# Optimization experiments

Hardware: AMD Instinct MI355X
Metric: run time of the kernel (lower is better)

The kernel has to match this reference:

```python
import jax, jax.numpy as jnp
import numpy as np

E, H = 1024, 16
HD = E // H
QLEN, KLEN, BS = 1024, 2048, 4
PREV = KLEN - QLEN


def _rel_shift(x):
    # x: (q, k, b, h) -> Transformer-XL relative shift
    q, k, b, h = x.shape
    x = jnp.pad(x, ((0, 0), (1, 0), (0, 0), (0, 0)))  # (q, k+1, b, h)
    x = x.reshape(k + 1, q, b, h)[1:].reshape(q, k, b, h)
    return x


def setup_inputs() -> dict:
    key = jax.random.key(0)
    ks = jax.random.split(key, 16)
    s = 0.02  # weight init scale
    inp = {
        "query": jax.random.normal(ks[0], (QLEN, BS, E), jnp.float32),
        "key": jax.random.normal(ks[1], (KLEN, BS, E), jnp.float32),
        "value": jax.random.normal(ks[2], (KLEN, BS, E), jnp.float32),
        "pos_embedding": jax.random.normal(ks[3], (KLEN, 1, E), jnp.float32),
        "U": jax.random.normal(ks[4], (H, HD), jnp.float32) * s,
        "V": jax.random.normal(ks[5], (H, HD), jnp.float32) * s,
        "Wq": jax.random.normal(ks[6], (E, E), jnp.float32) * s,
        "bq": jnp.zeros((E,), jnp.float32),
        "Wk": jax.random.normal(ks[7], (E, E), jnp.float32) * s,
        "bk": jnp.zeros((E,), jnp.float32),
        "Wv": jax.random.normal(ks[8], (E, E), jnp.float32) * s,
        "bv": jnp.zeros((E,), jnp.float32),
        "Wp": jax.random.normal(ks[9], (E, E), jnp.float32) * s,
        "Wo": jax.random.normal(ks[10], (E, E), jnp.float32) * s,
        "bo": jnp.zeros((E,), jnp.float32),
    }
    # causal XL mask: query i attends to keys j <= i + PREV; True = masked
    qi = jnp.arange(QLEN)[:, None]
    kj = jnp.arange(KLEN)[None, :]
    inp["mask"] = (kj > qi + PREV)[:, :, None]  # (q, k, 1) bool
    return inp


def reference(query, key, value, pos_embedding, U, V, Wq, bq, Wk, bk, Wv, bv, Wp, Wo, bo, mask):
    q_len, b, e = query.shape
    k_len = key.shape[0]
    scale = float(np.sqrt(e))  # note: sqrt(embed_dim), as in the source

    queries = (query @ Wq + bq).reshape(q_len, b, H, HD)
    keys = (key @ Wk + bk).reshape(k_len, b, H, HD)
    values = (value @ Wv + bv).reshape(k_len, b, H, HD)
    R = (pos_embedding @ Wp).reshape(-1, H, HD)  # (k, H, HD)

    content_score = jnp.einsum('qbhd,kbhd->qkbh', queries + U, keys)
    position_score = jnp.einsum('qbhd,khd->qkbh', queries + V, R)
    position_score = _rel_shift(position_score)

    attention_score = (content_score + position_score) / scale
    attention_score = jnp.where(mask[..., None], jnp.float32(-1e20), attention_score)
    attention = jax.nn.softmax(attention_score, axis=1)

    alpha = jnp.einsum('qkbh,kbhd->qbhd', attention, values).reshape(q_len, b, e)
    return alpha @ Wo + bo
```

## Files before the change

### kernel.cpp

```cpp
#include <hip/hip_runtime.h>
#include <stdint.h>

#define QLEN 1024
#define KLEN 2048
#define BSZ  4
#define NH   16
#define HD   64
#define EMB  1024
#define PREVL 1024
#define SLOG2E 0.045084220027780106f

typedef __attribute__((ext_vector_type(4))) float f32x4;
typedef __attribute__((ext_vector_type(8))) short bf16x8;

__device__ __forceinline__ unsigned short f2bf(float f){
  unsigned u = __float_as_uint(f);
  u += 0x7fffu + ((u >> 16) & 1u);
  return (unsigned short)(u >> 16);
}

__device__ __forceinline__ void gload_lds16(const void* g, void* l){
  __builtin_amdgcn_global_load_lds((const __attribute__((address_space(1))) void*)g,
                                   (__attribute__((address_space(3))) void*)l, 16, 0, 0);
}

__global__ void txl_prep(const float* __restrict__ w0, const float* __restrict__ w1,
                         const float* __restrict__ w2, const float* __restrict__ w3,
                         const float* __restrict__ w4,
                         unsigned short* __restrict__ o0, unsigned short* __restrict__ o1,
                         unsigned short* __restrict__ o2, unsigned short* __restrict__ o3,
                         unsigned short* __restrict__ o4,
                         const float* __restrict__ q, const float* __restrict__ k,
                         const float* __restrict__ v, const float* __restrict__ p,
                         unsigned short* __restrict__ qo, unsigned short* __restrict__ ko,
                         unsigned short* __restrict__ vo, unsigned short* __restrict__ po){
  const int bid = blockIdx.x;
  if (bid < 5120){
    const int z = bid >> 10, rem = bid & 1023;
    const int by = rem >> 5, bx = rem & 31;
    const float* in; unsigned short* out;
    switch (z){
      case 0: in = w0; out = o0; break;
      case 1: in = w1; out = o1; break;
      case 2: in = w2; out = o2; break;
      case 3: in = w3; out = o3; break;
      default: in = w4; out = o4; break;
    }
    __shared__ float tile[32][33];
    int tx = threadIdx.x & 31, ty = threadIdx.x >> 5;
    int k0 = by * 32, n0 = bx * 32;
    #pragma unroll
    for (int j = 0; j < 32; j += 8)
      tile[ty + j][tx] = in[(size_t)(k0 + ty + j) * EMB + n0 + tx];
    __syncthreads();
    #pragma unroll
    for (int j = 0; j < 32; j += 8)
      out[(size_t)(n0 + ty + j) * EMB + k0 + tx] = f2bf(tile[tx][ty + j]);
  } else {
    for (size_t c = (size_t)(bid - 5120) * 256 + threadIdx.x; c < 2883584; c += (size_t)2048 * 256){
      const float* src; unsigned short* dst; size_t off;
      if (c < 524288)      { src = q; dst = qo; off = c; }
      else if (c < 1572864){ src = k; dst = ko; off = c - 524288; }
      else if (c < 2621440){ src = v; dst = vo; off = c - 1572864; }
      else                 { src = p; dst = po; off = c - 2621440; }
      f32x4 a = *(const f32x4*)(src + off * 8);
      f32x4 b = *(const f32x4*)(src + off * 8 + 4);
      bf16x8 r;
      #pragma unroll
      for (int u = 0; u < 4; ++u){ r[u] = (short)f2bf(a[u]); r[u + 4] = (short)f2bf(b[u]); }
      *(bf16x8*)(dst + off * 8) = r;
    }
  }
}

__global__ __launch_bounds__(256)
void txl_gemm_proj(const unsigned short* __restrict__ pbf, const unsigned short* __restrict__ qbf,
                   const unsigned short* __restrict__ kbf, const unsigned short* __restrict__ vbf,
                   const unsigned short* __restrict__ WpT, const unsigned short* __restrict__ WqT,
                   const unsigned short* __restrict__ WkT, const unsigned short* __restrict__ WvT,
                   const float* __restrict__ bq, const float* __restrict__ bk,
                   const float* __restrict__ bv, const float* __restrict__ U,
                   const float* __restrict__ V,
                   unsigned short* __restrict__ Rb, unsigned short* __restrict__ Qu,
                   unsigned short* __restrict__ Qv, unsigned short* __restrict__ Kb,
                   unsigned short* __restrict__ Vt){
  const int bid = blockIdx.x;
  int mode, local;
  const unsigned short *Ag, *Wt;
  if (bid < 128)      { mode = 3; local = bid;       Ag = pbf; Wt = WpT; }
  else if (bid < 384) { mode = 0; local = bid - 128; Ag = qbf; Wt = WqT; }
  else if (bid < 896) { mode = 1; local = bid - 384; Ag = kbf; Wt = WkT; }
  else                { mode = 2; local = bid - 896; Ag = vbf; Wt = WvT; }
  const int m0 = (local >> 3) * 128, n0 = (local & 7) * 128;

  const int tid = threadIdx.x;
  const int lane = tid & 63, wave = tid >> 6;
  const int lr = lane & 15, lg = lane >> 4;
  const int wm = wave >> 1, wn = wave & 1;
  __shared__ union {
    struct { unsigned short At[128 * 64]; unsigned short Bt[128 * 64]; } ab;
    unsigned short tr[64 * 136];
  } smem;
  unsigned short* At = smem.ab.At;
  unsigned short* Bt = smem.ab.Bt;
  f32x4 acc[4][4] = {};

  for (int kt = 0; kt < EMB / 64; ++kt){
    const int k0 = kt * 64;
    __syncthreads();
    #pragma unroll
    for (int j = 0; j < 4; ++j){
      int row = j * 32 + (tid >> 3);
      int g = (tid & 7) ^ (row & 7);
      gload_lds16(Ag + (size_t)(m0 + row) * EMB + k0 + g * 8, &At[j * 2048 + wave * 512]);
      gload_lds16(Wt + (size_t)(n0 + row) * EMB + k0 + g * 8, &Bt[j * 2048 + wave * 512]);
    }
    __syncthreads();
    #pragma unroll
    for (int ks = 0; ks < 2; ++ks){
      bf16x8 af[4], bfr[4];
      #pragma unroll
      for (int mb = 0; mb < 4; ++mb){
        int row = wm * 64 + mb * 16 + lr;
        af[mb] = *(const bf16x8*)&At[row * 64 + ((lg + 4 * ks) ^ (row & 7)) * 8];
      }
      #pragma unroll
      for (int nb = 0; nb < 4; ++nb){
        int row = wn * 64 + nb * 16 + lr;
        bfr[nb] = *(const bf16x8*)&Bt[row * 64 + ((lg + 4 * ks) ^ (row & 7)) * 8];
      }
      __builtin_amdgcn_s_setprio(1);
      #pragma unroll
      for (int mb = 0; mb < 4; ++mb)
        #pragma unroll
        for (int nb = 0; nb < 4; ++nb)
          acc[mb][nb] = __builtin_amdgcn_mfma_f32_16x16x32_bf16(af[mb], bfr[nb], acc[mb][nb], 0, 0, 0);
      __builtin_amdgcn_s_setprio(0);
    }
  }

  if (mode == 2){
    const int kp0 = m0 >> 2;
    __syncthreads();
    #pragma unroll
    for (int pass = 0; pass < 2; ++pass){
      if (wn == pass){
        #pragma unroll
        for (int mb = 0; mb < 4; ++mb){
          int kp_l = wm * 16 + mb * 4 + lg;
          #pragma unroll
          for (int nb = 0; nb < 4; ++nb){
            int nl = nb * 16 + lr;
            float bvv = bv[n0 + pass * 64 + nl];
            #pragma unroll
            for (int i = 0; i < 4; ++i)
              smem.tr[nl * 136 + i * 32 + kp_l] = f2bf(acc[mb][nb][i] + bvv);
          }
        }
      }
      __syncthreads();
      #pragma unroll
      for (int it = 0; it < 4; ++it){
        int c = it * 256 + tid;
        int nl = c >> 4, bb = (c >> 2) & 3, kpc = c & 3;
        int n = n0 + pass * 64 + nl;
        int hh = n >> 6, dd = n & 63;
        bf16x8 vv = *(const bf16x8*)&smem.tr[nl * 136 + bb * 32 + kpc * 8];
        *(bf16x8*)&Vt[((((size_t)bb * NH + hh) * HD) + dd) * KLEN + kp0 + kpc * 8] = vv;
      }
      __syncthreads();
    }
  } else {
    #pragma unroll
    for (int mb = 0; mb < 4; ++mb){
      #pragma unroll
      for (int nb = 0; nb < 4; ++nb){
        #pragma unroll
        for (int i = 0; i < 4; ++i){
          int m = m0 + wm * 64 + mb * 16 + 4 * lg + i;
          int n = n0 + wn * 64 + nb * 16 + lr;
          float v = acc[mb][nb][i];
          if (mode == 0){
            int qq = m >> 2, b = m & 3, h = n >> 6, d = n & 63;
            size_t idx = ((((size_t)b * NH + h) * QLEN) + qq) * HD + d;
            float base = v + bq[n];
            Qu[idx] = f2bf((base + U[n]) * SLOG2E);
            Qv[idx] = f2bf((base + V[n]) * SLOG2E);
          } else if (mode == 1){
            int kp = m >> 2, b = m & 3, h = n >> 6, d = n & 63;
            Kb[((((size_t)b * NH + h) * KLEN) + kp) * HD + d] = f2bf(v + bk[n]);
          } else {
            int h = n >> 6, d = n & 63;
            Rb[((size_t)h * KLEN + m) * HD + d] = f2bf(v);
          }
        }
      }
    }
  }
}

__global__ __launch_bounds__(256)
void txl_gemm_out(const unsigned short* __restrict__ Ag, const unsigned short* __restrict__ Wt,
                  const float* __restrict__ bias, float* __restrict__ out0){
  const int tid = threadIdx.x;
  const int lane = tid & 63, wave = tid >> 6;
  const int lr = lane & 15, lg = lane >> 4;
  const int wm = wave >> 1, wn = wave & 1;
  const int m0 = blockIdx.y * 128, n0 = blockIdx.x * 128;
  __shared__ unsigned short At[128 * 64];
  __shared__ unsigned short Bt[128 * 64];
  f32x4 acc[4][4] = {};

  for (int kt = 0; kt < EMB / 64; ++kt){
    const int k0 = kt * 64;
    __syncthreads();
    #pragma unroll
    for (int j = 0; j < 4; ++j){
      int row = j * 32 + (tid >> 3);
      int g = (tid & 7) ^ (row & 7);
      gload_lds16(Ag + (size_t)(m0 + row) * EMB + k0 + g * 8, &At[j * 2048 + wave * 512]);
      gload_lds16(Wt + (size_t)(n0 + row) * EMB + k0 + g * 8, &Bt[j * 2048 + wave * 512]);
    }
    __syncthreads();
    #pragma unroll
    for (int ks = 0; ks < 2; ++ks){
      bf16x8 af[4], bfr[4];
      #pragma unroll
      for (int mb = 0; mb < 4; ++mb){
        int row = wm * 64 + mb * 16 + lr;
        af[mb] = *(const bf16x8*)&At[row * 64 + ((lg + 4 * ks) ^ (row & 7)) * 8];
      }
      #pragma unroll
      for (int nb = 0; nb < 4; ++nb){
        int row = wn * 64 + nb * 16 + lr;
        bfr[nb] = *(const bf16x8*)&Bt[row * 64 + ((lg + 4 * ks) ^ (row & 7)) * 8];
      }
      __builtin_amdgcn_s_setprio(1);
      #pragma unroll
      for (int mb = 0; mb < 4; ++mb)
        #pragma unroll
        for (int nb = 0; nb < 4; ++nb)
          acc[mb][nb] = __builtin_amdgcn_mfma_f32_16x16x32_bf16(af[mb], bfr[nb], acc[mb][nb], 0, 0, 0);
      __builtin_amdgcn_s_setprio(0);
    }
  }
  #pragma unroll
  for (int mb = 0; mb < 4; ++mb)
    #pragma unroll
    for (int nb = 0; nb < 4; ++nb)
      #pragma unroll
      for (int i = 0; i < 4; ++i){
        int m = m0 + wm * 64 + mb * 16 + 4 * lg + i;
        int n = n0 + wn * 64 + nb * 16 + lr;
        out0[(size_t)m * EMB + n] = acc[mb][nb][i] + bias[n];
      }
}

__global__ __launch_bounds__(256)
void txl_attn(const unsigned short* __restrict__ Qu, const unsigned short* __restrict__ Qv,
              const unsigned short* __restrict__ Kb, const unsigned short* __restrict__ Vt,
              const unsigned short* __restrict__ Rb, unsigned short* __restrict__ alpha){
  const int tid = threadIdx.x, lane = tid & 63, wave = tid >> 6;
  const int lr = lane & 15, lg = lane >> 4;
  const int qt = 15 - blockIdx.x;
  const int h = blockIdx.y, b = blockIdx.z;
  const int q0 = qt * 64;
  const int myq0 = q0 + 16 * wave;

  __shared__ union { unsigned short q[2][64 * 64]; unsigned short p[4][16 * 64]; } smq;
  __shared__ unsigned short sm_k[64 * 64];
  __shared__ unsigned short sm_v[64 * 64];
  __shared__ unsigned short sm_r[128 * 64];
  __shared__ float sm_t[4][16 * 81];

  const unsigned short* quB = Qu + (((size_t)b * NH + h) * QLEN) * HD;
  const unsigned short* qvB = Qv + (((size_t)b * NH + h) * QLEN) * HD;
  const unsigned short* kB  = Kb + (((size_t)b * NH + h) * KLEN) * HD;
  const unsigned short* vB  = Vt + (((size_t)b * NH + h) * HD) * KLEN;
  const unsigned short* rB  = Rb + ((size_t)h * KLEN) * HD;

  #pragma unroll
  for (int j = 0; j < 2; ++j){
    int row = j * 32 + (tid >> 3);
    int g = (tid & 7) ^ (row & 7);
    gload_lds16(quB + (size_t)(q0 + row) * HD + g * 8, &smq.q[0][j * 2048 + wave * 512]);
    gload_lds16(qvB + (size_t)(q0 + row) * HD + g * 8, &smq.q[1][j * 2048 + wave * 512]);
  }
  const int rbase0 = (QLEN - 64) - q0;
  #pragma unroll
  for (int j = 0; j < 4; ++j){
    int S = rbase0 + j * 32;
    int rs = S + (tid >> 3);
    int g = (tid & 7) ^ (rs & 7);
    gload_lds16(rB + (size_t)rs * HD + g * 8, &sm_r[(S & 127) * 64 + wave * 512]);
  }
  __syncthreads();
  bf16x8 qfu[2], qfv[2];
  {
    int row = 16 * wave + lr;
    #pragma unroll
    for (int ks = 0; ks < 2; ++ks){
      qfu[ks] = *(const bf16x8*)&smq.q[0][row * 64 + ((lg + 4 * ks) ^ (row & 7)) * 8];
      qfv[ks] = *(const bf16x8*)&smq.q[1][row * 64 + ((lg + 4 * ks) ^ (row & 7)) * 8];
    }
  }

  f32x4 o[4] = {};
  float ls[4] = {0.f, 0.f, 0.f, 0.f};

  const int nk = qt + 17;
  const int roff = 48 - 16 * wave;

  for (int kt = 0; kt < nk; ++kt){
    const int k0 = kt * 64;
    const int rbase = k0 + (QLEN - 64) - q0;
    const int roff64 = rbase & 64;
    __syncthreads();
    #pragma unroll
    for (int j = 0; j < 2; ++j){
      int row = j * 32 + (tid >> 3);
      int g = (tid & 7) ^ (row & 7);
      gload_lds16(kB + (size_t)(k0 + row) * HD + g * 8, &sm_k[j * 2048 + wave * 512]);
      gload_lds16(vB + (size_t)row * KLEN + k0 + g * 8, &sm_v[j * 2048 + wave * 512]);
    }
    if (kt > 0){
      #pragma unroll
      for (int j = 0; j < 2; ++j){
        int S = rbase + 64 + j * 32;
        int rs = S + (tid >> 3);
        int rc = rs < KLEN - 1 ? rs : KLEN - 1;
        int g = (tid & 7) ^ (rs & 7);
        gload_lds16(rB + (size_t)rc * HD + g * 8, &sm_r[(S & 127) * 64 + wave * 512]);
      }
    }
    __syncthreads();

    f32x4 sc[4] = {};
    f32x4 tt[5] = {};
    __builtin_amdgcn_s_setprio(1);
    #pragma unroll
    for (int ks = 0; ks < 2; ++ks){
      #pragma unroll
      for (int nb = 0; nb < 4; ++nb){
        int row = nb * 16 + lr;
        bf16x8 kf = *(const bf16x8*)&sm_k[row * 64 + ((lg + 4 * ks) ^ (row & 7)) * 8];
        sc[nb] = __builtin_amdgcn_mfma_f32_16x16x32_bf16(qfu[ks], kf, sc[nb], 0, 0, 0);
      }
      #pragma unroll
      for (int rb = 0; rb < 5; ++rb){
        int row = roff + rb * 16 + lr;
        int slot = row ^ roff64;
        bf16x8 rf = *(const bf16x8*)&sm_r[slot * 64 + ((lg + 4 * ks) ^ (row & 7)) * 8];
        tt[rb] = __builtin_amdgcn_mfma_f32_16x16x32_bf16(qfv[ks], rf, tt[rb], 0, 0, 0);
      }
    }
    __builtin_amdgcn_s_setprio(0);

    float* tw = sm_t[wave];
    #pragma unroll
    for (int rb = 0; rb < 5; ++rb)
      #pragma unroll
      for (int i = 0; i < 4; ++i)
        tw[(4 * lg + i) * 81 + rb * 16 + lr] = tt[rb][i];
    asm volatile("s_waitcnt lgkmcnt(0)" ::: "memory");

    if (kt + 1 < nk){
      #pragma unroll
      for (int i = 0; i < 4; ++i){
        int qq = 4 * lg + i;
        float rs = 0.f;
        #pragma unroll
        for (int nb = 0; nb < 4; ++nb){
          int kk = nb * 16 + lr;
          float p = exp2f(sc[nb][i] + tw[qq * 81 + kk + 15 - qq]);
          rs += p;
          smq.p[wave][qq * 64 + (((kk >> 3) ^ (qq & 7)) << 3) + (kk & 7)] = f2bf(p);
        }
        ls[i] += rs;
      }
    } else {
      #pragma unroll
      for (int i = 0; i < 4; ++i){
        int qq = 4 * lg + i;
        int qglob = myq0 + qq;
        float rs = 0.f;
        #pragma unroll
        for (int nb = 0; nb < 4; ++nb){
          int kk = nb * 16 + lr;
          float s = sc[nb][i] + tw[qq * 81 + kk + 15 - qq];
          if (k0 + kk > qglob + PREVL) s = -1e30f;
          float p = exp2f(s);
          rs += p;
          smq.p[wave][qq * 64 + (((kk >> 3) ^ (qq & 7)) << 3) + (kk & 7)] = f2bf(p);
        }
        ls[i] += rs;
      }
    }
    asm volatile("s_waitcnt lgkmcnt(0)" ::: "memory");

    __builtin_amdgcn_s_setprio(1);
    #pragma unroll
    for (int ks = 0; ks < 2; ++ks){
      bf16x8 pa = *(const bf16x8*)&smq.p[wave][lr * 64 + ((lg + 4 * ks) ^ (lr & 7)) * 8];
      #pragma unroll
      for (int db = 0; db < 4; ++db){
        int row = db * 16 + lr;
        bf16x8 vf = *(const bf16x8*)&sm_v[row * 64 + ((lg + 4 * ks) ^ (row & 7)) * 8];
        o[db] = __builtin_amdgcn_mfma_f32_16x16x32_bf16(pa, vf, o[db], 0, 0, 0);
      }
    }
    __builtin_amdgcn_s_setprio(0);
  }

  #pragma unroll
  for (int i = 0; i < 4; ++i){
    float s = ls[i];
    s += __shfl_xor(s, 1); s += __shfl_xor(s, 2);
    s += __shfl_xor(s, 4); s += __shfl_xor(s, 8);
    float inv = 1.0f / s;
    int q = myq0 + 4 * lg + i;
    #pragma unroll
    for (int db = 0; db < 4; ++db){
      int e = (h << 6) + db * 16 + lr;
      alpha[((size_t)q * BSZ + b) * EMB + e] = f2bf(o[db][i] * inv);
    }
  }
}

extern "C" void kernel_launch(void* const* d_in, const int* in_sizes, int n_in,
                              void* d_out, int out_size, void* d_ws, size_t ws_size,
                              hipStream_t stream) {
  const float* query = (const float*)d_in[0];
  const float* key   = (const float*)d_in[1];
  const float* value = (const float*)d_in[2];
  const float* pos   = (const float*)d_in[3];
  const float* U     = (const float*)d_in[4];
  const float* V     = (const float*)d_in[5];
  const float* Wq    = (const float*)d_in[6];
  const float* bq    = (const float*)d_in[7];
  const float* Wk    = (const float*)d_in[8];
  const float* bk    = (const float*)d_in[9];
  const float* Wv    = (const float*)d_in[10];
  const float* bv    = (const float*)d_in[11];
  const float* Wp    = (const float*)d_in[12];
  const float* Wo    = (const float*)d_in[13];
  const float* bo    = (const float*)d_in[14];

  char* w = (char*)d_ws;
  const size_t MB = 1u << 20;
  unsigned short* WqT = (unsigned short*)(w + 0 * MB);
  unsigned short* WkT = (unsigned short*)(w + 2 * MB);
  unsigned short* WvT = (unsigned short*)(w + 4 * MB);
  unsigned short* WpT = (unsigned short*)(w + 6 * MB);
  unsigned short* WoT = (unsigned short*)(w + 8 * MB);
  unsigned short* Qu  = (unsigned short*)(w + 10 * MB);
  unsigned short* Qv  = (unsigned short*)(w + 18 * MB);
  unsigned short* Kb  = (unsigned short*)(w + 26 * MB);
  unsigned short* Vt  = (unsigned short*)(w + 42 * MB);
  unsigned short* Rb  = (unsigned short*)(w + 58 * MB);
  unsigned short* qbf = (unsigned short*)(w + 62 * MB);
  unsigned short* kbf = (unsigned short*)(w + 70 * MB);
  unsigned short* vbf = (unsigned short*)(w + 86 * MB);
  unsigned short* pbf = (unsigned short*)(w + 102 * MB);
  unsigned short* alpha = qbf;

  txl_prep<<<dim3(7168), 256, 0, stream>>>(Wq, Wk, Wv, Wp, Wo, WqT, WkT, WvT, WpT, WoT,
                                           query, key, value, pos, qbf, kbf, vbf, pbf);

  txl_gemm_proj<<<dim3(1408), 256, 0, stream>>>(pbf, qbf, kbf, vbf, WpT, WqT, WkT, WvT,
                                                bq, bk, bv, U, V, Rb, Qu, Qv, Kb, Vt);

  txl_attn<<<dim3(16, 16, 4), 256, 0, stream>>>(Qu, Qv, Kb, Vt, Rb, alpha);

  txl_gemm_out<<<dim3(8, 32), 256, 0, stream>>>(alpha, WoT, bo, (float*)d_out);
}
```

Measured before the change: 264.2 us.

## Double-buffer K/V tiles, ring-buffer R, and store position scores as bf16

Measured after the change: 276.8 us. +4.8%, slower.

```diff
diff --git a/kernel.cpp b/kernel.cpp
--- a/kernel.cpp
+++ b/kernel.cpp
@@ -9,6 +9,7 @@
 #define EMB  1024
 #define PREVL 1024
 #define SLOG2E 0.045084220027780106f
+#define TPAD 83
 
 typedef __attribute__((ext_vector_type(4))) float f32x4;
 typedef __attribute__((ext_vector_type(8))) short bf16x8;
@@ -17,6 +18,12 @@
   unsigned u = __float_as_uint(f);
   u += 0x7fffu + ((u >> 16) & 1u);
   return (unsigned short)(u >> 16);
+}
+__device__ __forceinline__ unsigned short f2bf_trunc(float f){
+  return (unsigned short)(__float_as_uint(f) >> 16);
+}
+__device__ __forceinline__ float bf2f(unsigned short s){
+  return __uint_as_float(((unsigned)s) << 16);
 }
 
 __device__ __forceinline__ void gload_lds16(const void* g, void* l){
@@ -267,11 +274,11 @@
   const int q0 = qt * 64;
   const int myq0 = q0 + 16 * wave;
 
-  __shared__ union { unsigned short q[2][64 * 64]; unsigned short p[4][16 * 64]; } smq;
-  __shared__ unsigned short sm_k[64 * 64];
-  __shared__ unsigned short sm_v[64 * 64];
-  __shared__ unsigned short sm_r[128 * 64];
-  __shared__ float sm_t[4][16 * 81];
+  __shared__ unsigned short sm_p[4][16 * 64];
+  __shared__ unsigned short sm_k[2][64 * 64];
+  __shared__ unsigned short sm_v[2][64 * 64];
+  __shared__ unsigned short sm_r[192 * 64];
+  __shared__ unsigned short sm_t[4][16 * TPAD];
 
   const unsigned short* quB = Qu + (((size_t)b * NH + h) * QLEN) * HD;
   const unsigned short* qvB = Qv + (((size_t)b * NH + h) * QLEN) * HD;
@@ -279,62 +286,74 @@
   const unsigned short* vB  = Vt + (((size_t)b * NH + h) * HD) * KLEN;
   const unsigned short* rB  = Rb + ((size_t)h * KLEN) * HD;
 
+  const int nk = qt + 17;
+  const int roff = 48 - 16 * wave;
+  const int rbase0 = (QLEN - 64) - q0;
+
   #pragma unroll
   for (int j = 0; j < 2; ++j){
     int row = j * 32 + (tid >> 3);
     int g = (tid & 7) ^ (row & 7);
-    gload_lds16(quB + (size_t)(q0 + row) * HD + g * 8, &smq.q[0][j * 2048 + wave * 512]);
-    gload_lds16(qvB + (size_t)(q0 + row) * HD + g * 8, &smq.q[1][j * 2048 + wave * 512]);
-  }
-  const int rbase0 = (QLEN - 64) - q0;
-  #pragma unroll
-  for (int j = 0; j < 4; ++j){
-    int S = rbase0 + j * 32;
-    int rs = S + (tid >> 3);
-    int g = (tid & 7) ^ (rs & 7);
-    gload_lds16(rB + (size_t)rs * HD + g * 8, &sm_r[(S & 127) * 64 + wave * 512]);
-  }
-  __syncthreads();
+    gload_lds16(kB + (size_t)row * HD + g * 8, &sm_k[0][j * 2048 + wave * 512]);
+    gload_lds16(vB + (size_t)row * KLEN + g * 8, &sm_v[0][j * 2048 + wave * 512]);
+  }
+  {
+    int b192 = rbase0 % 192;
+    #pragma unroll
+    for (int j = 0; j < 4; ++j){
+      int S = rbase0 + j * 32;
+      int rs = S + (tid >> 3);
+      int g = (tid & 7) ^ (rs & 7);
+      int slotS = b192 + j * 32; if (slotS >= 192) slotS -= 192;
+      gload_lds16(rB + (size_t)rs * HD + g * 8, &sm_r[slotS * 64 + wave * 512]);
+    }
+  }
   bf16x8 qfu[2], qfv[2];
   {
-    int row = 16 * wave + lr;
+    int qrow = myq0 + lr;
     #pragma unroll
     for (int ks = 0; ks < 2; ++ks){
-      qfu[ks] = *(const bf16x8*)&smq.q[0][row * 64 + ((lg + 4 * ks) ^ (row & 7)) * 8];
-      qfv[ks] = *(const bf16x8*)&smq.q[1][row * 64 + ((lg + 4 * ks) ^ (row & 7)) * 8];
+      qfu[ks] = *(const bf16x8*)(quB + (size_t)qrow * HD + (lg + 4 * ks) * 8);
+      qfv[ks] = *(const bf16x8*)(qvB + (size_t)qrow * HD + (lg + 4 * ks) * 8);
     }
   }
 
   f32x4 o[4] = {};
   float ls[4] = {0.f, 0.f, 0.f, 0.f};
 
-  const int nk = qt + 17;
-  const int roff = 48 - 16 * wave;
-
   for (int kt = 0; kt < nk; ++kt){
     const int k0 = kt * 64;
-    const int rbase = k0 + (QLEN - 64) - q0;
-    const int roff64 = rbase & 64;
-    __syncthreads();
-    #pragma unroll
-    for (int j = 0; j < 2; ++j){
-      int row = j * 32 + (tid >> 3);
-      int g = (tid & 7) ^ (row & 7);
-      gload_lds16(kB + (size_t)(k0 + row) * HD + g * 8, &sm_k[j * 2048 + wave * 512]);
-      gload_lds16(vB + (size_t)row * KLEN + k0 + g * 8, &sm_v[j * 2048 + wave * 512]);
-    }
-    if (kt > 0){
+    const int rbase = k0 + rbase0;
+    const int b192 = rbase % 192;
+    const int cur = kt & 1;
+    __syncthreads();
+
+    if (kt + 1 < nk){
+      const int nxt = cur ^ 1;
       #pragma unroll
       for (int j = 0; j < 2; ++j){
-        int S = rbase + 64 + j * 32;
+        int row = j * 32 + (tid >> 3);
+        int g = (tid & 7) ^ (row & 7);
+        gload_lds16(kB + (size_t)(k0 + 64 + row) * HD + g * 8, &sm_k[nxt][j * 2048 + wave * 512]);
+        gload_lds16(vB + (size_t)row * KLEN + (k0 + 64) + g * 8, &sm_v[nxt][j * 2048 + wave * 512]);
+      }
+      #pragma unroll
+      for (int j = 0; j < 2; ++j){
+        int S = rbase + 128 + j * 32;
         int rs = S + (tid >> 3);
         int rc = rs < KLEN - 1 ? rs : KLEN - 1;
         int g = (tid & 7) ^ (rs & 7);
-        gload_lds16(rB + (size_t)rc * HD + g * 8, &sm_r[(S & 127) * 64 + wave * 512]);
-      }
-    }
-    __syncthreads();
-
+        int slotS = b192 + 128 + j * 32; if (slotS >= 192) slotS -= 192;
+        gload_lds16(rB + (size_t)rc * HD + g * 8, &sm_r[slotS * 64 + wave * 512]);
+      }
+    }
+
+    int slotb[5];
+    #pragma unroll
+    for (int rb = 0; rb < 5; ++rb){
+      int s = b192 + roff + rb * 16; if (s >= 192) s -= 192;
+      slotb[rb] = s;
+    }
     f32x4 sc[4] = {};
     f32x4 tt[5] = {};
     __builtin_amdgcn_s_setprio(1);
@@ -343,25 +362,24 @@
       #pragma unroll
       for (int nb = 0; nb < 4; ++nb){
         int row = nb * 16 + lr;
-        bf16x8 kf = *(const bf16x8*)&sm_k[row * 64 + ((lg + 4 * ks) ^ (row & 7)) * 8];
+        bf16x8 kf = *(const bf16x8*)&sm_k[cur][row * 64 + ((lg + 4 * ks) ^ (row & 7)) * 8];
         sc[nb] = __builtin_amdgcn_mfma_f32_16x16x32_bf16(qfu[ks], kf, sc[nb], 0, 0, 0);
       }
       #pragma unroll
       for (int rb = 0; rb < 5; ++rb){
-        int row = roff + rb * 16 + lr;
-        int slot = row ^ roff64;
-        bf16x8 rf = *(const bf16x8*)&sm_r[slot * 64 + ((lg + 4 * ks) ^ (row & 7)) * 8];
+        int s = slotb[rb] + lr; if (s >= 192) s -= 192;
+        bf16x8 rf = *(const bf16x8*)&sm_r[s * 64 + ((lg + 4 * ks) ^ (lr & 7)) * 8];
         tt[rb] = __builtin_amdgcn_mfma_f32_16x16x32_bf16(qfv[ks], rf, tt[rb], 0, 0, 0);
       }
     }
     __builtin_amdgcn_s_setprio(0);
 
-    float* tw = sm_t[wave];
+    unsigned short* tw = sm_t[wave];
     #pragma unroll
     for (int rb = 0; rb < 5; ++rb)
       #pragma unroll
       for (int i = 0; i < 4; ++i)
-        tw[(4 * lg + i) * 81 + rb * 16 + lr] = tt[rb][i];
+        tw[(4 * lg + i) * TPAD + rb * 16 + lr] = f2bf_trunc(tt[rb][i]);
     asm volatile("s_waitcnt lgkmcnt(0)" ::: "memory");
 
     if (kt + 1 < nk){
@@ -372,9 +390,9 @@
         #pragma unroll
         for (int nb = 0; nb < 4; ++nb){
           int kk = nb * 16 + lr;
-          float p = exp2f(sc[nb][i] + tw[qq * 81 + kk + 15 - qq]);
+          float p = exp2f(sc[nb][i] + bf2f(tw[qq * TPAD + kk + 15 - qq]));
           rs += p;
-          smq.p[wave][qq * 64 + (((kk >> 3) ^ (qq & 7)) << 3) + (kk & 7)] = f2bf(p);
+          sm_p[wave][qq * 64 + (((kk >> 3) ^ (qq & 7)) << 3) + (kk & 7)] = f2bf(p);
         }
         ls[i] += rs;
       }
@@ -387,11 +405,11 @@
         #pragma unroll
         for (int nb = 0; nb < 4; ++nb){
           int kk = nb * 16 + lr;
-          float s = sc[nb][i] + tw[qq * 81 + kk + 15 - qq];
+          float s = sc[nb][i] + bf2f(tw[qq * TPAD + kk + 15 - qq]);
           if (k0 + kk > qglob + PREVL) s = -1e30f;
           float p = exp2f(s);
           rs += p;
-          smq.p[wave][qq * 64 + (((kk >> 3) ^ (qq & 7)) << 3) + (kk & 7)] = f2bf(p);
+          sm_p[wave][qq * 64 + (((kk >> 3) ^ (qq & 7)) << 3) + (kk & 7)] = f2bf(p);
         }
         ls[i] += rs;
       }
@@ -401,11 +419,11 @@
     __builtin_amdgcn_s_setprio(1);
     #pragma unroll
     for (int ks = 0; ks < 2; ++ks){
-      bf16x8 pa = *(const bf16x8*)&smq.p[wave][lr * 64 + ((lg + 4 * ks) ^ (lr & 7)) * 8];
+      bf16x8 pa = *(const bf16x8*)&sm_p[wave][lr * 64 + ((lg + 4 * ks) ^ (lr & 7)) * 8];
       #pragma unroll
       for (int db = 0; db < 4; ++db){
         int row = db * 16 + lr;
-        bf16x8 vf = *(const bf16x8*)&sm_v[row * 64 + ((lg + 4 * ks) ^ (row & 7)) * 8];
+        bf16x8 vf = *(const bf16x8*)&sm_v[cur][row * 64 + ((lg + 4 * ks) ^ (row & 7)) * 8];
         o[db] = __builtin_amdgcn_mfma_f32_16x16x32_bf16(pa, vf, o[db], 0, 0, 0);
       }
     }
```
